# Kernel tuning notes

Measured on AMD Instinct MI355X. Metric: run time of the kernel, lower is better.

Reference implementation:

```python
import jax, jax.numpy as jnp
import numpy as np
from jax import lax

EPS = 1e-5  # BatchNorm eps (inference mode: running_mean=m, running_var=v)
DN = ('NCDHW', 'OIDHW', 'NCDHW')


def _conv_bn_relu(x, W, b, g, bt, m, v, pad):
    y = lax.conv_general_dilated(x, W, window_strides=(1, 1, 1), padding=pad,
                                 dimension_numbers=DN)
    y = y + b[None, :, None, None, None]
    scale = g / jnp.sqrt(v + EPS)
    y = (y - m[None, :, None, None, None]) * scale[None, :, None, None, None] \
        + bt[None, :, None, None, None]
    return jax.nn.relu(y)


def _cal_patt(k, q, v):
    # spatial non-local attention over H*W, independently per (n, c, d)
    N, C, D, H, W = q.shape
    qf = q.reshape(N, C, D, H * W)
    kf = k.reshape(N, C, D, H * W)
    vf = v.reshape(N, C, D, H * W)
    # sigma[n,c,d,i,j] = q_i * k_j ; softmax over j ; out[j] = sum_i v_i * r_ij
    sigma = qf[..., :, None] * kf[..., None, :]          # [N,C,D,HW,HW]
    r = jax.nn.softmax(sigma, axis=-1)
    out = jnp.einsum('ncdi,ncdij->ncdj', vf, r)
    return out.reshape(N, C, D, H, W)


def _cal_datt(k, q, v):
    # temporal non-local attention over D, independently per (n, c, h, w)
    N, C, D, H, W = q.shape
    qf = jnp.transpose(q, (0, 1, 3, 4, 2))               # [N,C,H,W,D]
    kf = jnp.transpose(k, (0, 1, 3, 4, 2))
    vf = jnp.transpose(v, (0, 1, 3, 4, 2))
    sigma = qf[..., :, None] * kf[..., None, :]          # [N,C,H,W,D,D]
    r = jax.nn.softmax(sigma, axis=-1)
    out = jnp.einsum('nchwi,nchwij->nchwj', vf, r)
    return jnp.transpose(out, (0, 1, 4, 2, 3))           # back to [N,C,D,H,W]


def setup_inputs() -> dict:
    key = jax.random.key(0)
    ks = jax.random.split(key, 8)
    C, Cc = 512, 64  # features_, features_//compress
    N, D, H, W = 2, 8, 16, 16
    f32 = jnp.float32

    def bn(c):
        return (jnp.ones((c,), f32), jnp.zeros((c,), f32),
                jnp.zeros((c,), f32), jnp.ones((c,), f32))

    x = jax.random.normal(ks[0], (N, C, D, H, W), f32)
    Wq = jax.random.normal(ks[1], (Cc, C, 1, 1, 1), f32) * 0.04
    Wk = jax.random.normal(ks[2], (Cc, C, 1, 1, 1), f32) * 0.04
    Wv = jax.random.normal(ks[3], (Cc, C, 1, 1, 1), f32) * 0.04
    Ws = jax.random.normal(ks[4], (C, Cc, 3, 3, 3), f32) * 0.02
    Wd = jax.random.normal(ks[5], (C, Cc, 3, 3, 3), f32) * 0.02
    gq, btq, mq, vq = bn(Cc)
    gk, btk, mk, vk = bn(Cc)
    gv, btv, mv, vv = bn(Cc)
    gs, bts, ms, vs = bn(C)
    gd, btd, md, vd = bn(C)
    return dict(
        x=x, gama=jnp.float32(0.5),
        Wq=Wq, bq=jnp.zeros((Cc,), f32), gq=gq, btq=btq, mq=mq, vq=vq,
        Wk=Wk, bk=jnp.zeros((Cc,), f32), gk=gk, btk=btk, mk=mk, vk=vk,
        Wv=Wv, bv=jnp.zeros((Cc,), f32), gv=gv, btv=btv, mv=mv, vv=vv,
        Ws=Ws, bs=jnp.zeros((C,), f32), gs=gs, bts=bts, ms=ms, vs=vs,
        Wd=Wd, bd=jnp.zeros((C,), f32), gd=gd, btd=btd, md=md, vd=vd,
    )


def reference(x, gama,
              Wq, bq, gq, btq, mq, vq,
              Wk, bk, gk, btk, mk, vk,
              Wv, bv, gv, btv, mv, vv,
              Ws, bs, gs, bts, ms, vs,
              Wd, bd, gd, btd, md, vd):
    P0 = [(0, 0)] * 3
    P1 = [(1, 1)] * 3
    v_x = _conv_bn_relu(x, Wv, bv, gv, btv, mv, vv, P0)
    k_x = _conv_bn_relu(x, Wk, bk, gk, btk, mk, vk, P0)
    q_x = _conv_bn_relu(x, Wq, bq, gq, btq, mq, vq, P0)
    # name == 'st': both spatial and temporal attention branches
    Patt = _cal_patt(k_x, q_x, v_x)
    Patt_c = _conv_bn_relu(Patt, Ws, bs, gs, bts, ms, vs, P1)
    Datt = _cal_datt(k_x, q_x, v_x)
    Datt_c = _conv_bn_relu(Datt, Wd, bd, gd, btd, md, vd, P1)
    return gama * (Datt_c + Patt_c) + x
```

## Files before the change

kernel.cpp:

```cpp
#include <hip/hip_runtime.h>
#include <cmath>

#define EPSBN 1e-5f

namespace {
constexpr int C_IN = 512;
constexpr int CC   = 64;
constexpr int CD   = 8;
constexpr int HW   = 256;
constexpr int DHW  = CD * HW;
constexpr int QSZ  = 2 * CC * DHW;

constexpr int PG    = 18 * 18;
constexpr int GPLN  = PG * 8;
constexpr int PADSZ = 2 * 10 * 8 * GPLN;
constexpr int WTSZ  = 27 * 512 * 64;

typedef __attribute__((ext_vector_type(8))) short bf16x8;
typedef __attribute__((ext_vector_type(4))) float f32x4;
typedef __attribute__((ext_vector_type(16))) float f32x16;

typedef unsigned int u32_g __attribute__((address_space(1)));
typedef unsigned int u32_l __attribute__((address_space(3)));

__device__ inline unsigned short f2bf(float f) {
    unsigned u = __float_as_uint(f);
    return (unsigned short)((u + 0x7fffu + ((u >> 16) & 1u)) >> 16);
}
}

__global__ __launch_bounds__(256) void prep_kernel(
    const float* __restrict__ Ws, const float* __restrict__ Wd,
    const float* __restrict__ Wq, const float* __restrict__ Wk,
    const float* __restrict__ Wv,
    const float* __restrict__ bs, const float* __restrict__ gs,
    const float* __restrict__ bts, const float* __restrict__ ms,
    const float* __restrict__ vs,
    const float* __restrict__ bd, const float* __restrict__ gd,
    const float* __restrict__ btd, const float* __restrict__ md,
    const float* __restrict__ vd,
    uint4* __restrict__ pads, unsigned short* __restrict__ Wt,
    unsigned short* __restrict__ Wqkv, float2* __restrict__ BNc)
{
    int bid = blockIdx.x;
    int t = threadIdx.x;
    if (bid < 405) {
        pads[bid * 256 + t] = make_uint4(0, 0, 0, 0);
    } else if (bid < 1429) {
        int b2 = bid - 405;
        int b  = b2 >> 9;
        int co = b2 & 511;
        const float* W = b ? Wd : Ws;
        int cog = co >> 6, co_l = co & 63;
        int r  = co_l & 31, hi = co_l >> 5;
        unsigned short* o = Wt + (size_t)b * WTSZ;
        for (int k = t; k < 27 * 64; k += 256) {
            int tap = k >> 6, ci = k & 63;
            int kd = tap / 9, tapk = tap - kd * 9;
            int half = ci >> 5, cl = ci & 31;
            int cig = cl >> 4, ci16 = cl & 15;
            int ks = ci16 >> 3;
            float w = W[((size_t)co * 64 + ci) * 27 + tap];
            int chunk = ((cog * 2 + half) * 3 + kd) * 2 + cig;
            int pg = (r * 2 + ks) ^ (r & 7);
            o[(size_t)chunk * 9216 + tapk * 1024 + hi * 512
              + pg * 8 + (ci16 & 7)] = f2bf(w);
        }
    } else if (bid < 1621) {
        int co = bid - 1429;
        const float* W = co < 64 ? Wq : co < 128 ? Wk : Wv;
        int c = co & 63;
        for (int ci = t; ci < 512; ci += 256)
            Wqkv[(size_t)co * 512 + ci] = f2bf(W[(size_t)c * 512 + ci]);
    } else {
        int gid = (bid - 1621) * 256 + t;
        if (gid < 1024) {
            int br = gid >> 9, co = gid & 511;
            float s, o;
            if (br == 0) {
                s = gs[co] * rsqrtf(vs[co] + EPSBN);
                o = (bs[co] - ms[co]) * s + bts[co];
            } else {
                s = gd[co] * rsqrtf(vd[co] + EPSBN);
                o = (bd[co] - md[co]) * s + btd[co];
            }
            BNc[gid] = make_float2(s, o);
        }
    }
}

__global__ __launch_bounds__(256) void qkv_gemm_kernel(
    const float* __restrict__ x, const unsigned short* __restrict__ Wqkv,
    const float* __restrict__ bq, const float* __restrict__ gq,
    const float* __restrict__ btq, const float* __restrict__ mq,
    const float* __restrict__ vq,
    const float* __restrict__ bk, const float* __restrict__ gk,
    const float* __restrict__ btk, const float* __restrict__ mk,
    const float* __restrict__ vk,
    const float* __restrict__ bv, const float* __restrict__ gv,
    const float* __restrict__ btv, const float* __restrict__ mv,
    const float* __restrict__ vv,
    float* __restrict__ outq, float* __restrict__ outk, float* __restrict__ outv)
{
    int bid = blockIdx.x;
    int n = bid >> 7, p0 = (bid & 127) * 16;

    __shared__ __align__(16) unsigned short xs[16 * 512];
    int t = threadIdx.x;

    const float* xb = x + ((size_t)n * C_IN) * DHW + p0;
#pragma unroll
    for (int pass = 0; pass < 8; ++pass) {
        int idx = pass * 256 + t;
        int ci = idx >> 2, pq = idx & 3;
        float4 v4 = *reinterpret_cast<const float4*>(xb + (size_t)ci * DHW + pq * 4);
        float arr[4] = {v4.x, v4.y, v4.z, v4.w};
#pragma unroll
        for (int u = 0; u < 4; ++u) {
            int pos = pq * 4 + u;
            int boff = pos * 1024 + ((ci * 2) ^ ((pos & 7) << 4));
            *reinterpret_cast<unsigned short*>(
                reinterpret_cast<char*>(xs) + boff) = f2bf(arr[u]);
        }
    }
    __syncthreads();

    int wid = t >> 6, lane = t & 63;
    int l15 = lane & 15, l4 = lane >> 4;
    int mh = wid * 3;
    int pos = l15;

    bf16x8 bfr[16];
    const char* xsb = reinterpret_cast<const char*>(xs) + pos * 1024;
    int swz = (pos & 7) << 4;
#pragma unroll
    for (int kk = 0; kk < 16; ++kk)
        bfr[kk] = *reinterpret_cast<const bf16x8*>(xsb + ((kk * 64 + l4 * 16) ^ swz));

    f32x4 acc[3];
#pragma unroll
    for (int i = 0; i < 3; ++i) acc[i] = (f32x4){0.f, 0.f, 0.f, 0.f};

#pragma unroll
    for (int i = 0; i < 3; ++i) {
        const unsigned short* wrow =
            Wqkv + ((size_t)(mh + i) * 16 + l15) * 512 + l4 * 8;
#pragma unroll
        for (int kk = 0; kk < 16; ++kk) {
            bf16x8 af = *reinterpret_cast<const bf16x8*>(wrow + kk * 32);
            acc[i] = __builtin_amdgcn_mfma_f32_16x16x32_bf16(af, bfr[kk], acc[i], 0, 0, 0);
        }
    }

#pragma unroll
    for (int i = 0; i < 3; ++i) {
        int mf = mh + i;
        int br = mf >> 2;
        const float* bb  = br == 0 ? bq  : br == 1 ? bk  : bv;
        const float* gg  = br == 0 ? gq  : br == 1 ? gk  : gv;
        const float* bt  = br == 0 ? btq : br == 1 ? btk : btv;
        const float* mm  = br == 0 ? mq  : br == 1 ? mk  : mv;
        const float* vvp = br == 0 ? vq  : br == 1 ? vk  : vv;
        float*       op  = br == 0 ? outq : br == 1 ? outk : outv;
        int cb = (mf & 3) * 16 + l4 * 4;
#pragma unroll
        for (int r = 0; r < 4; ++r) {
            int c = cb + r;
            float s = gg[c] * rsqrtf(vvp[c] + EPSBN);
            float val = (acc[i][r] + bb[c] - mm[c]) * s + bt[c];
            op[((size_t)(n * CC + c)) * DHW + p0 + pos] = fmaxf(val, 0.f);
        }
    }
}

__global__ __launch_bounds__(256) void att_kernel(
    const float* __restrict__ q, const float* __restrict__ k,
    const float* __restrict__ v,
    unsigned short* __restrict__ Pp, unsigned short* __restrict__ Dp)
{
    __shared__ float sk[256], sq[256], sw[256], red[4];
    int t = threadIdx.x;
    int bid = blockIdx.x;

    if (bid < 1024) {
        int n = bid >> 9, c = (bid >> 3) & 63, d = bid & 7;
        size_t base = (size_t)bid * HW;
        float kt = k[base + t];
        float qt = q[base + t];
        float vt = v[base + t];
        sk[t] = kt;
        sq[t] = qt;

        float m = kt;
#pragma unroll
        for (int off = 32; off >= 1; off >>= 1)
            m = fmaxf(m, __shfl_xor(m, off));
        if ((t & 63) == 0) red[t >> 6] = m;
        __syncthreads();
        float kmax = fmaxf(fmaxf(red[0], red[1]), fmaxf(red[2], red[3]));

        float qkm = qt * kmax;
        float d0 = 0.f, d1 = 0.f, d2 = 0.f, d3 = 0.f;
        for (int j = 0; j < 256; j += 4) {
            d0 += __expf(fmaf(qt, sk[j + 0], -qkm));
            d1 += __expf(fmaf(qt, sk[j + 1], -qkm));
            d2 += __expf(fmaf(qt, sk[j + 2], -qkm));
            d3 += __expf(fmaf(qt, sk[j + 3], -qkm));
        }
        float den = (d0 + d1) + (d2 + d3);
        sw[t] = vt / den;
        __syncthreads();

        float kjm = kt - kmax;
        float o0 = 0.f, o1 = 0.f, o2 = 0.f, o3 = 0.f;
        for (int i = 0; i < 256; i += 4) {
            o0 += sw[i + 0] * __expf(sq[i + 0] * kjm);
            o1 += sw[i + 1] * __expf(sq[i + 1] * kjm);
            o2 += sw[i + 2] * __expf(sq[i + 2] * kjm);
            o3 += sw[i + 3] * __expf(sq[i + 3] * kjm);
        }
        float o = (o0 + o1) + (o2 + o3);

        int h = t >> 4, w = t & 15;
        size_t dst = ((((size_t)(n * 10 + d + 1) * 8 + (c >> 3)) * PG)
                      + (h + 1) * 18 + (w + 1)) * 8 + (c & 7);
        Pp[dst] = f2bf(o);
    } else {
        int g = (bid - 1024) * 256 + t;
        int nc = g >> 8, hw = g & 255;
        int n = nc >> 6, c = nc & 63;
        size_t base = (size_t)nc * DHW + hw;

        float qv[8], kv[8], vv_[8];
#pragma unroll
        for (int d = 0; d < 8; ++d) {
            qv[d]  = q[base + d * HW];
            kv[d]  = k[base + d * HW];
            vv_[d] = v[base + d * HW];
        }
        float kmax = 0.f;
#pragma unroll
        for (int d = 0; d < 8; ++d) kmax = fmaxf(kmax, kv[d]);

        float wgt[8];
#pragma unroll
        for (int i = 0; i < 8; ++i) {
            float den = 0.f, qkm = qv[i] * kmax;
#pragma unroll
            for (int j = 0; j < 8; ++j)
                den += __expf(fmaf(qv[i], kv[j], -qkm));
            wgt[i] = vv_[i] / den;
        }
        int h = hw >> 4, w = hw & 15;
#pragma unroll
        for (int j = 0; j < 8; ++j) {
            float o = 0.f, kjm = kv[j] - kmax;
#pragma unroll
            for (int i = 0; i < 8; ++i)
                o += wgt[i] * __expf(qv[i] * kjm);
            size_t dst = ((((size_t)(n * 10 + j + 1) * 8 + (c >> 3)) * PG)
                          + (h + 1) * 18 + (w + 1)) * 8 + (c & 7);
            Dp[dst] = f2bf(o);
        }
    }
}

__global__ __launch_bounds__(256, 1) void conv_fused_kernel(
    const unsigned short* __restrict__ Pp, const unsigned short* __restrict__ Dp,
    const unsigned short* __restrict__ Wt,
    const float2* __restrict__ BNc,
    const float* __restrict__ x, const float* __restrict__ gama,
    float* __restrict__ out)
{
    int bid = blockIdx.x;
    int cog = bid & 7;
    int pgb = (bid >> 3) & 1;
    int sl  = bid >> 4;
    int n = sl >> 3, d = sl & 7;

    __shared__ __align__(16) unsigned short lds_in[24 * 1536];
    __shared__ __align__(16) unsigned short lds_w[2 * 18432];

    int t = threadIdx.x;
    int wid = t >> 6, lane = t & 63;
    int ph = wid & 1, br = wid >> 1;
    int col  = lane & 31;
    int wcol = lane & 15;
    int hl   = (lane >> 4) & 1;
    int ks   = lane >> 5;
    int gA   = ((col * 2 + ks) ^ (col & 7)) * 8;

    f32x16 acc[2][2];
#pragma unroll
    for (int m = 0; m < 2; ++m)
#pragma unroll
        for (int p = 0; p < 2; ++p)
#pragma unroll
            for (int r = 0; r < 16; ++r)
                acc[m][p][r] = 0.f;

#define ISTAGE(hf_) do {                                                      \
    _Pragma("unroll")                                                         \
    for (int pc = 0; pc < 24; ++pc) {                                         \
        const unsigned short* sb = ((pc >= 12) ? Dp : Pp)                     \
            + ((size_t)((n * 10 + d + ((pc % 12) >> 2)) * 8 + (hf_) * 4       \
                        + ((pc % 12) & 3))) * GPLN + pgb * 1152;              \
        _Pragma("unroll")                                                     \
        for (int j = 0; j < 3; ++j) {                                         \
            if (((pc * 3 + j) & 3) == wid)                                    \
                __builtin_amdgcn_global_load_lds(                             \
                    (const u32_g*)(sb + j * 512 + lane * 8),                  \
                    (u32_l*)(lds_in + pc * 1536 + j * 512), 16, 0, 0);        \
        }                                                                     \
    }                                                                         \
} while (0)

#define DMAW(c_) do {                                                         \
    const int ch_ = (((cog * 2 + ((c_) / 6)) * 3 + (((c_) % 6) >> 1)) * 2     \
                     + ((c_) & 1)) * 9216;                                    \
    _Pragma("unroll")                                                         \
    for (int j = 0; j < 9; ++j) {                                             \
        int base = j * 2048 + wid * 512;                                      \
        const unsigned short* s0 = (base < 9216)                              \
            ? (Wt + ch_ + base)                                               \
            : (Wt + WTSZ + ch_ + (base - 9216));                              \
        __builtin_amdgcn_global_load_lds(                                     \
            (const u32_g*)(s0 + lane * 8),                                    \
            (u32_l*)(lds_w + ((c_) & 1) * 18432 + base), 16, 0, 0);           \
    }                                                                         \
} while (0)

#define COMPUTE(c_) do {                                                      \
    const int kd_ = ((c_) % 6) >> 1, cig_ = (c_) & 1;                         \
    const unsigned short* wb_ = lds_w + ((c_) & 1) * 18432 + br * 9216;       \
    const unsigned short* bp_ = lds_in + br * (12 * 1536)                     \
                                + (kd_ * 4 + cig_ * 2 + ks) * 1536;           \
    _Pragma("unroll")                                                         \
    for (int tapk = 0; tapk < 9; ++tapk) {                                    \
        const int kh_ = tapk / 3, kw_ = tapk % 3;                             \
        bf16x8 a0 = *(const bf16x8*)(wb_ + tapk * 1024 + gA);                 \
        bf16x8 a1 = *(const bf16x8*)(wb_ + tapk * 1024 + 512 + gA);           \
        bf16x8 b0 = *(const bf16x8*)(bp_ + ((ph * 4 + hl + kh_) * 18          \
                                     + wcol + kw_) * 8);                      \
        bf16x8 b1 = *(const bf16x8*)(bp_ + ((ph * 4 + 2 + hl + kh_) * 18      \
                                     + wcol + kw_) * 8);                      \
        acc[0][0] = __builtin_amdgcn_mfma_f32_32x32x16_bf16(a0, b0,           \
                        acc[0][0], 0, 0, 0);                                  \
        acc[0][1] = __builtin_amdgcn_mfma_f32_32x32x16_bf16(a0, b1,           \
                        acc[0][1], 0, 0, 0);                                  \
        acc[1][0] = __builtin_amdgcn_mfma_f32_32x32x16_bf16(a1, b0,           \
                        acc[1][0], 0, 0, 0);                                  \
        acc[1][1] = __builtin_amdgcn_mfma_f32_32x32x16_bf16(a1, b1,           \
                        acc[1][1], 0, 0, 0);                                  \
    }                                                                         \
} while (0)

    ISTAGE(0);
    DMAW(0);
    __syncthreads();

#pragma unroll
    for (int c = 0; c < 12; ++c) {
        if (c < 11) DMAW(c + 1);
        COMPUTE(c);
        __syncthreads();
        if (c == 5) {
            ISTAGE(1);
            __syncthreads();
        }
    }

#undef ISTAGE
#undef DMAW
#undef COMPUTE

    float gm = gama[0];
    float* ep = reinterpret_cast<float*>(lds_w);

    if (br == 0) {
#pragma unroll
        for (int m = 0; m < 2; ++m)
#pragma unroll
            for (int p = 0; p < 2; ++p)
#pragma unroll
                for (int r = 0; r < 16; ++r) {
                    int row = (r & 3) + 8 * (r >> 2) + 4 * ks;
                    float2 c2 = BNc[cog * 64 + m * 32 + row];
                    float v = fmaxf(acc[m][p][r] * c2.x + c2.y, 0.f);
                    ep[ph * 4096 + (m * 32 + row) * 64 + p * 32 + col] = v;
                }
    }
    __syncthreads();
    if (br == 1) {
#pragma unroll
        for (int m = 0; m < 2; ++m)
#pragma unroll
            for (int p = 0; p < 2; ++p)
#pragma unroll
                for (int r = 0; r < 16; ++r) {
                    int row = (r & 3) + 8 * (r >> 2) + 4 * ks;
                    int co = cog * 64 + m * 32 + row;
                    float2 c2 = BNc[512 + co];
                    float rd = fmaxf(acc[m][p][r] * c2.x + c2.y, 0.f);
                    float rp = ep[ph * 4096 + (m * 32 + row) * 64 + p * 32 + col];
                    int pos = pgb * 128 + ph * 64 + p * 32 + col;
                    size_t oi = ((size_t)(n * 512 + co)) * 2048 + d * 256 + pos;
                    out[oi] = gm * (rp + rd) + x[oi];
                }
    }
}

extern "C" void kernel_launch(void* const* d_in, const int* in_sizes, int n_in,
                              void* d_out, int out_size, void* d_ws, size_t ws_size,
                              hipStream_t stream)
{
    const float* x    = (const float*)d_in[0];
    const float* gama = (const float*)d_in[1];
    const float* Wq  = (const float*)d_in[2];
    const float* bq  = (const float*)d_in[3];
    const float* gq  = (const float*)d_in[4];
    const float* btq = (const float*)d_in[5];
    const float* mq  = (const float*)d_in[6];
    const float* vq  = (const float*)d_in[7];
    const float* Wk  = (const float*)d_in[8];
    const float* bk  = (const float*)d_in[9];
    const float* gk  = (const float*)d_in[10];
    const float* btk = (const float*)d_in[11];
    const float* mk  = (const float*)d_in[12];
    const float* vk  = (const float*)d_in[13];
    const float* Wv  = (const float*)d_in[14];
    const float* bv  = (const float*)d_in[15];
    const float* gv  = (const float*)d_in[16];
    const float* btv = (const float*)d_in[17];
    const float* mv  = (const float*)d_in[18];
    const float* vv  = (const float*)d_in[19];
    const float* Ws  = (const float*)d_in[20];
    const float* bs  = (const float*)d_in[21];
    const float* gs  = (const float*)d_in[22];
    const float* bts = (const float*)d_in[23];
    const float* ms  = (const float*)d_in[24];
    const float* vs  = (const float*)d_in[25];
    const float* Wd  = (const float*)d_in[26];
    const float* bd  = (const float*)d_in[27];
    const float* gd  = (const float*)d_in[28];
    const float* btd = (const float*)d_in[29];
    const float* md  = (const float*)d_in[30];
    const float* vd  = (const float*)d_in[31];

    char* ws = (char*)d_ws;
    unsigned short* Pp   = (unsigned short*)ws;
    unsigned short* Dp   = Pp + PADSZ;
    unsigned short* Wt   = Dp + PADSZ;
    unsigned short* Wqkv = Wt + 2 * WTSZ;
    float* q = (float*)(ws + 5394432);
    float* k = q + QSZ;
    float* v = k + QSZ;
    float2* BNc = (float2*)(ws + 5394432 + 3 * 1048576);

    prep_kernel<<<1625, 256, 0, stream>>>(
        Ws, Wd, Wq, Wk, Wv,
        bs, gs, bts, ms, vs,
        bd, gd, btd, md, vd,
        (uint4*)Pp, Wt, Wqkv, BNc);

    qkv_gemm_kernel<<<256, 256, 0, stream>>>(
        x, Wqkv,
        bq, gq, btq, mq, vq,
        bk, gk, btk, mk, vk,
        bv, gv, btv, mv, vv,
        q, k, v);

    att_kernel<<<1152, 256, 0, stream>>>(q, k, v, Pp, Dp);

    conv_fused_kernel<<<256, 256, 0, stream>>>(
        Pp, Dp, Wt, BNc,
        x, gama, (float*)d_out);
}
```

Before: 65.02 us.

## Double-buffer conv input staging per chunk and vectorize attention LDS reads

The fused conv kernel no longer stages a whole half of the input planes (24 planes) at once with an extra barrier mid-loop. It now double-buffers a small 4-plane input slice per chunk alongside the weight DMA, which shrinks LDS use from about 72KB to 24KB for inputs and removes the stall at chunk 5. The attention kernel reads its shared k/q/w arrays as float4 with partial unrolling, and the weight-prep loop now reads source weights contiguously. The risk is more frequent small DMA issues per iteration, which could add latency if the per-chunk loads are not hidden behind compute.

```diff
diff --git a/kernel.cpp b/kernel.cpp
--- a/kernel.cpp
+++ b/kernel.cpp
@@ -54,13 +54,14 @@
         int cog = co >> 6, co_l = co & 63;
         int r  = co_l & 31, hi = co_l >> 5;
         unsigned short* o = Wt + (size_t)b * WTSZ;
-        for (int k = t; k < 27 * 64; k += 256) {
-            int tap = k >> 6, ci = k & 63;
+        for (int k2 = t; k2 < 27 * 64; k2 += 256) {
+            int ci  = k2 / 27;
+            int tap = k2 - ci * 27;
             int kd = tap / 9, tapk = tap - kd * 9;
             int half = ci >> 5, cl = ci & 31;
             int cig = cl >> 4, ci16 = cl & 15;
             int ks = ci16 >> 3;
-            float w = W[((size_t)co * 64 + ci) * 27 + tap];
+            float w = W[(size_t)co * 1728 + k2];
             int chunk = ((cog * 2 + half) * 3 + kd) * 2 + cig;
             int pg = (r * 2 + ks) ^ (r & 7);
             o[(size_t)chunk * 9216 + tapk * 1024 + hi * 512
@@ -178,7 +179,8 @@
     const float* __restrict__ v,
     unsigned short* __restrict__ Pp, unsigned short* __restrict__ Dp)
 {
-    __shared__ float sk[256], sq[256], sw[256], red[4];
+    __shared__ __align__(16) float sk[256], sq[256], sw[256];
+    __shared__ float red[4];
     int t = threadIdx.x;
     int bid = blockIdx.x;
 
@@ -201,11 +203,14 @@
 
         float qkm = qt * kmax;
         float d0 = 0.f, d1 = 0.f, d2 = 0.f, d3 = 0.f;
-        for (int j = 0; j < 256; j += 4) {
-            d0 += __expf(fmaf(qt, sk[j + 0], -qkm));
-            d1 += __expf(fmaf(qt, sk[j + 1], -qkm));
-            d2 += __expf(fmaf(qt, sk[j + 2], -qkm));
-            d3 += __expf(fmaf(qt, sk[j + 3], -qkm));
+        const float4* sk4 = reinterpret_cast<const float4*>(sk);
+#pragma unroll 8
+        for (int j = 0; j < 64; ++j) {
+            float4 kk = sk4[j];
+            d0 += __expf(fmaf(qt, kk.x, -qkm));
+            d1 += __expf(fmaf(qt, kk.y, -qkm));
+            d2 += __expf(fmaf(qt, kk.z, -qkm));
+            d3 += __expf(fmaf(qt, kk.w, -qkm));
         }
         float den = (d0 + d1) + (d2 + d3);
         sw[t] = vt / den;
@@ -213,11 +218,16 @@
 
         float kjm = kt - kmax;
         float o0 = 0.f, o1 = 0.f, o2 = 0.f, o3 = 0.f;
-        for (int i = 0; i < 256; i += 4) {
-            o0 += sw[i + 0] * __expf(sq[i + 0] * kjm);
-            o1 += sw[i + 1] * __expf(sq[i + 1] * kjm);
-            o2 += sw[i + 2] * __expf(sq[i + 2] * kjm);
-            o3 += sw[i + 3] * __expf(sq[i + 3] * kjm);
+        const float4* sw4 = reinterpret_cast<const float4*>(sw);
+        const float4* sq4 = reinterpret_cast<const float4*>(sq);
+#pragma unroll 8
+        for (int i = 0; i < 64; ++i) {
+            float4 ww = sw4[i];
+            float4 qq = sq4[i];
+            o0 += ww.x * __expf(qq.x * kjm);
+            o1 += ww.y * __expf(qq.y * kjm);
+            o2 += ww.z * __expf(qq.z * kjm);
+            o3 += ww.w * __expf(qq.w * kjm);
         }
         float o = (o0 + o1) + (o2 + o3);
 
@@ -278,7 +288,7 @@
     int sl  = bid >> 4;
     int n = sl >> 3, d = sl & 7;
 
-    __shared__ __align__(16) unsigned short lds_in[24 * 1536];
+    __shared__ __align__(16) unsigned short lds_i[8 * 1536];
     __shared__ __align__(16) unsigned short lds_w[2 * 18432];
 
     int t = threadIdx.x;
@@ -299,18 +309,21 @@
             for (int r = 0; r < 16; ++r)
                 acc[m][p][r] = 0.f;
 
-#define ISTAGE(hf_) do {                                                      \
+#define DMAI(c_) do {                                                         \
+    const int half_ = (c_) / 6, kd_ = (((c_) % 6) >> 1), cig_ = (c_) & 1;     \
     _Pragma("unroll")                                                         \
-    for (int pc = 0; pc < 24; ++pc) {                                         \
-        const unsigned short* sb = ((pc >= 12) ? Dp : Pp)                     \
-            + ((size_t)((n * 10 + d + ((pc % 12) >> 2)) * 8 + (hf_) * 4       \
-                        + ((pc % 12) & 3))) * GPLN + pgb * 1152;              \
+    for (int pc = 0; pc < 4; ++pc) {                                          \
+        const int br_ = pc >> 1, ks_ = pc & 1;                                \
+        const unsigned short* sb = (br_ ? Dp : Pp)                            \
+            + ((size_t)((n * 10 + d + kd_) * 8 + half_ * 4 + cig_ * 2 + ks_)) \
+              * GPLN + pgb * 1152;                                            \
         _Pragma("unroll")                                                     \
         for (int j = 0; j < 3; ++j) {                                         \
             if (((pc * 3 + j) & 3) == wid)                                    \
                 __builtin_amdgcn_global_load_lds(                             \
                     (const u32_g*)(sb + j * 512 + lane * 8),                  \
-                    (u32_l*)(lds_in + pc * 1536 + j * 512), 16, 0, 0);        \
+                    (u32_l*)(lds_i + (((c_) & 1) * 4 + pc) * 1536 + j * 512), \
+                    16, 0, 0);                                                \
         }                                                                     \
     }                                                                         \
 } while (0)
@@ -331,10 +344,8 @@
 } while (0)
 
 #define COMPUTE(c_) do {                                                      \
-    const int kd_ = ((c_) % 6) >> 1, cig_ = (c_) & 1;                         \
     const unsigned short* wb_ = lds_w + ((c_) & 1) * 18432 + br * 9216;       \
-    const unsigned short* bp_ = lds_in + br * (12 * 1536)                     \
-                                + (kd_ * 4 + cig_ * 2 + ks) * 1536;           \
+    const unsigned short* bp_ = lds_i + (((c_) & 1) * 4 + br * 2 + ks) * 1536;\
     _Pragma("unroll")                                                         \
     for (int tapk = 0; tapk < 9; ++tapk) {                                    \
         const int kh_ = tapk / 3, kw_ = tapk % 3;                             \
@@ -355,22 +366,21 @@
     }                                                                         \
 } while (0)
 
-    ISTAGE(0);
+    DMAI(0);
     DMAW(0);
     __syncthreads();
 
 #pragma unroll
     for (int c = 0; c < 12; ++c) {
-        if (c < 11) DMAW(c + 1);
+        if (c < 11) {
+            DMAW(c + 1);
+            DMAI(c + 1);
+        }
         COMPUTE(c);
         __syncthreads();
-        if (c == 5) {
-            ISTAGE(1);
-            __syncthreads();
-        }
-    }
-
-#undef ISTAGE
+    }
+
+#undef DMAI
 #undef DMAW
 #undef COMPUTE
 
```

Measured after the change: 67.56 us. 1.04x slower.

## Fuse weight prep and QKV GEMM into one head kernel, relax conv barriers

Applied to the files above, without the earlier changes.

Merges the prep and QKV projection kernels into a single launch. The QKV blocks now read the fp32 Wq/Wk/Wv weights directly and convert them to bf16 in registers, so the intermediate Wqkv buffer and one kernel launch go away. The conv weight repack loop is reordered so its global reads are contiguous. The conv pipeline replaces __syncthreads with raw s_barrier plus explicit vmcnt waits so that the next chunk's DMA can stay in flight. The risks are redundant weight conversion in every block and the correctness of the hand-tuned vmcnt count.

```diff
diff --git a/kernel.cpp b/kernel.cpp
--- a/kernel.cpp
+++ b/kernel.cpp
@@ -29,10 +29,20 @@
 }
 }
 
-__global__ __launch_bounds__(256) void prep_kernel(
-    const float* __restrict__ Ws, const float* __restrict__ Wd,
+__global__ __launch_bounds__(256) void head_kernel(
+    const float* __restrict__ x,
     const float* __restrict__ Wq, const float* __restrict__ Wk,
     const float* __restrict__ Wv,
+    const float* __restrict__ bq, const float* __restrict__ gq,
+    const float* __restrict__ btq, const float* __restrict__ mq,
+    const float* __restrict__ vq,
+    const float* __restrict__ bk, const float* __restrict__ gk,
+    const float* __restrict__ btk, const float* __restrict__ mk,
+    const float* __restrict__ vk,
+    const float* __restrict__ bv, const float* __restrict__ gv,
+    const float* __restrict__ btv, const float* __restrict__ mv,
+    const float* __restrict__ vv,
+    const float* __restrict__ Ws, const float* __restrict__ Wd,
     const float* __restrict__ bs, const float* __restrict__ gs,
     const float* __restrict__ bts, const float* __restrict__ ms,
     const float* __restrict__ vs,
@@ -40,40 +50,114 @@
     const float* __restrict__ btd, const float* __restrict__ md,
     const float* __restrict__ vd,
     uint4* __restrict__ pads, unsigned short* __restrict__ Wt,
-    unsigned short* __restrict__ Wqkv, float2* __restrict__ BNc)
+    float2* __restrict__ BNc,
+    float* __restrict__ outq, float* __restrict__ outk, float* __restrict__ outv)
 {
     int bid = blockIdx.x;
     int t = threadIdx.x;
-    if (bid < 405) {
-        pads[bid * 256 + t] = make_uint4(0, 0, 0, 0);
-    } else if (bid < 1429) {
-        int b2 = bid - 405;
+
+    if (bid < 256) {
+        int n = bid >> 7, p0 = (bid & 127) * 16;
+
+        __shared__ __align__(16) unsigned short xs[16 * 512];
+
+        const float* xb = x + ((size_t)n * C_IN) * DHW + p0;
+#pragma unroll
+        for (int pass = 0; pass < 8; ++pass) {
+            int idx = pass * 256 + t;
+            int ci = idx >> 2, pq = idx & 3;
+            float4 v4 = *reinterpret_cast<const float4*>(xb + (size_t)ci * DHW + pq * 4);
+            float arr[4] = {v4.x, v4.y, v4.z, v4.w};
+#pragma unroll
+            for (int u = 0; u < 4; ++u) {
+                int pos = pq * 4 + u;
+                int boff = pos * 1024 + ((ci * 2) ^ ((pos & 7) << 4));
+                *reinterpret_cast<unsigned short*>(
+                    reinterpret_cast<char*>(xs) + boff) = f2bf(arr[u]);
+            }
+        }
+        __syncthreads();
+
+        int wid = t >> 6, lane = t & 63;
+        int l15 = lane & 15, l4 = lane >> 4;
+        int mh = wid * 3;
+        int pos = l15;
+
+        bf16x8 bfr[16];
+        const char* xsb = reinterpret_cast<const char*>(xs) + pos * 1024;
+        int swz = (pos & 7) << 4;
+#pragma unroll
+        for (int kk = 0; kk < 16; ++kk)
+            bfr[kk] = *reinterpret_cast<const bf16x8*>(xsb + ((kk * 64 + l4 * 16) ^ swz));
+
+        f32x4 acc[3];
+#pragma unroll
+        for (int i = 0; i < 3; ++i) acc[i] = (f32x4){0.f, 0.f, 0.f, 0.f};
+
+#pragma unroll
+        for (int i = 0; i < 3; ++i) {
+            int mf = mh + i;
+            int br = mf >> 2;
+            const float* Wsel = br == 0 ? Wq : br == 1 ? Wk : Wv;
+            int c = (mf & 3) * 16 + l15;
+            const float* wr = Wsel + (size_t)c * 512 + l4 * 8;
+#pragma unroll
+            for (int kk = 0; kk < 16; ++kk) {
+                float4 wa = *reinterpret_cast<const float4*>(wr + kk * 32);
+                float4 wb = *reinterpret_cast<const float4*>(wr + kk * 32 + 4);
+                bf16x8 af;
+                af[0] = (short)f2bf(wa.x); af[1] = (short)f2bf(wa.y);
+                af[2] = (short)f2bf(wa.z); af[3] = (short)f2bf(wa.w);
+                af[4] = (short)f2bf(wb.x); af[5] = (short)f2bf(wb.y);
+                af[6] = (short)f2bf(wb.z); af[7] = (short)f2bf(wb.w);
+                acc[i] = __builtin_amdgcn_mfma_f32_16x16x32_bf16(af, bfr[kk], acc[i], 0, 0, 0);
+            }
+        }
+
+#pragma unroll
+        for (int i = 0; i < 3; ++i) {
+            int mf = mh + i;
+            int br = mf >> 2;
+            const float* bb  = br == 0 ? bq  : br == 1 ? bk  : bv;
+            const float* gg  = br == 0 ? gq  : br == 1 ? gk  : gv;
+            const float* bt  = br == 0 ? btq : br == 1 ? btk : btv;
+            const float* mm  = br == 0 ? mq  : br == 1 ? mk  : mv;
+            const float* vvp = br == 0 ? vq  : br == 1 ? vk  : vv;
+            float*       op  = br == 0 ? outq : br == 1 ? outk : outv;
+            int cb = (mf & 3) * 16 + l4 * 4;
+#pragma unroll
+            for (int r = 0; r < 4; ++r) {
+                int c = cb + r;
+                float s = gg[c] * rsqrtf(vvp[c] + EPSBN);
+                float val = (acc[i][r] + bb[c] - mm[c]) * s + bt[c];
+                op[((size_t)(n * CC + c)) * DHW + p0 + pos] = fmaxf(val, 0.f);
+            }
+        }
+    } else if (bid < 661) {
+        pads[(bid - 256) * 256 + t] = make_uint4(0, 0, 0, 0);
+    } else if (bid < 1685) {
+        int b2 = bid - 661;
         int b  = b2 >> 9;
         int co = b2 & 511;
         const float* W = b ? Wd : Ws;
         int cog = co >> 6, co_l = co & 63;
         int r  = co_l & 31, hi = co_l >> 5;
         unsigned short* o = Wt + (size_t)b * WTSZ;
-        for (int k = t; k < 27 * 64; k += 256) {
-            int tap = k >> 6, ci = k & 63;
+        for (int k2 = t; k2 < 27 * 64; k2 += 256) {
+            int ci  = k2 / 27;
+            int tap = k2 - ci * 27;
             int kd = tap / 9, tapk = tap - kd * 9;
             int half = ci >> 5, cl = ci & 31;
             int cig = cl >> 4, ci16 = cl & 15;
             int ks = ci16 >> 3;
-            float w = W[((size_t)co * 64 + ci) * 27 + tap];
+            float w = W[(size_t)co * 1728 + k2];
             int chunk = ((cog * 2 + half) * 3 + kd) * 2 + cig;
             int pg = (r * 2 + ks) ^ (r & 7);
             o[(size_t)chunk * 9216 + tapk * 1024 + hi * 512
               + pg * 8 + (ci16 & 7)] = f2bf(w);
         }
-    } else if (bid < 1621) {
-        int co = bid - 1429;
-        const float* W = co < 64 ? Wq : co < 128 ? Wk : Wv;
-        int c = co & 63;
-        for (int ci = t; ci < 512; ci += 256)
-            Wqkv[(size_t)co * 512 + ci] = f2bf(W[(size_t)c * 512 + ci]);
     } else {
-        int gid = (bid - 1621) * 256 + t;
+        int gid = (bid - 1685) * 256 + t;
         if (gid < 1024) {
             int br = gid >> 9, co = gid & 511;
             float s, o;
@@ -85,90 +169,6 @@
                 o = (bd[co] - md[co]) * s + btd[co];
             }
             BNc[gid] = make_float2(s, o);
-        }
-    }
-}
-
-__global__ __launch_bounds__(256) void qkv_gemm_kernel(
-    const float* __restrict__ x, const unsigned short* __restrict__ Wqkv,
-    const float* __restrict__ bq, const float* __restrict__ gq,
-    const float* __restrict__ btq, const float* __restrict__ mq,
-    const float* __restrict__ vq,
-    const float* __restrict__ bk, const float* __restrict__ gk,
-    const float* __restrict__ btk, const float* __restrict__ mk,
-    const float* __restrict__ vk,
-    const float* __restrict__ bv, const float* __restrict__ gv,
-    const float* __restrict__ btv, const float* __restrict__ mv,
-    const float* __restrict__ vv,
-    float* __restrict__ outq, float* __restrict__ outk, float* __restrict__ outv)
-{
-    int bid = blockIdx.x;
-    int n = bid >> 7, p0 = (bid & 127) * 16;
-
-    __shared__ __align__(16) unsigned short xs[16 * 512];
-    int t = threadIdx.x;
-
-    const float* xb = x + ((size_t)n * C_IN) * DHW + p0;
-#pragma unroll
-    for (int pass = 0; pass < 8; ++pass) {
-        int idx = pass * 256 + t;
-        int ci = idx >> 2, pq = idx & 3;
-        float4 v4 = *reinterpret_cast<const float4*>(xb + (size_t)ci * DHW + pq * 4);
-        float arr[4] = {v4.x, v4.y, v4.z, v4.w};
-#pragma unroll
-        for (int u = 0; u < 4; ++u) {
-            int pos = pq * 4 + u;
-            int boff = pos * 1024 + ((ci * 2) ^ ((pos & 7) << 4));
-            *reinterpret_cast<unsigned short*>(
-                reinterpret_cast<char*>(xs) + boff) = f2bf(arr[u]);
-        }
-    }
-    __syncthreads();
-
-    int wid = t >> 6, lane = t & 63;
-    int l15 = lane & 15, l4 = lane >> 4;
-    int mh = wid * 3;
-    int pos = l15;
-
-    bf16x8 bfr[16];
-    const char* xsb = reinterpret_cast<const char*>(xs) + pos * 1024;
-    int swz = (pos & 7) << 4;
-#pragma unroll
-    for (int kk = 0; kk < 16; ++kk)
-        bfr[kk] = *reinterpret_cast<const bf16x8*>(xsb + ((kk * 64 + l4 * 16) ^ swz));
-
-    f32x4 acc[3];
-#pragma unroll
-    for (int i = 0; i < 3; ++i) acc[i] = (f32x4){0.f, 0.f, 0.f, 0.f};
-
-#pragma unroll
-    for (int i = 0; i < 3; ++i) {
-        const unsigned short* wrow =
-            Wqkv + ((size_t)(mh + i) * 16 + l15) * 512 + l4 * 8;
-#pragma unroll
-        for (int kk = 0; kk < 16; ++kk) {
-            bf16x8 af = *reinterpret_cast<const bf16x8*>(wrow + kk * 32);
-            acc[i] = __builtin_amdgcn_mfma_f32_16x16x32_bf16(af, bfr[kk], acc[i], 0, 0, 0);
-        }
-    }
-
-#pragma unroll
-    for (int i = 0; i < 3; ++i) {
-        int mf = mh + i;
-        int br = mf >> 2;
-        const float* bb  = br == 0 ? bq  : br == 1 ? bk  : bv;
-        const float* gg  = br == 0 ? gq  : br == 1 ? gk  : gv;
-        const float* bt  = br == 0 ? btq : br == 1 ? btk : btv;
-        const float* mm  = br == 0 ? mq  : br == 1 ? mk  : mv;
-        const float* vvp = br == 0 ? vq  : br == 1 ? vk  : vv;
-        float*       op  = br == 0 ? outq : br == 1 ? outk : outv;
-        int cb = (mf & 3) * 16 + l4 * 4;
-#pragma unroll
-        for (int r = 0; r < 4; ++r) {
-            int c = cb + r;
-            float s = gg[c] * rsqrtf(vvp[c] + EPSBN);
-            float val = (acc[i][r] + bb[c] - mm[c]) * s + bt[c];
-            op[((size_t)(n * CC + c)) * DHW + p0 + pos] = fmaxf(val, 0.f);
         }
     }
 }
@@ -357,16 +357,22 @@
 
     ISTAGE(0);
     DMAW(0);
-    __syncthreads();
 
 #pragma unroll
     for (int c = 0; c < 12; ++c) {
-        if (c < 11) DMAW(c + 1);
+        if (c > 0)
+            __builtin_amdgcn_s_barrier();
+        if (c < 11) {
+            DMAW(c + 1);
+            asm volatile("s_waitcnt vmcnt(9)" ::: "memory");
+        } else {
+            asm volatile("s_waitcnt vmcnt(0)" ::: "memory");
+        }
+        __builtin_amdgcn_s_barrier();
         COMPUTE(c);
-        __syncthreads();
         if (c == 5) {
+            __builtin_amdgcn_s_barrier();
             ISTAGE(1);
-            __syncthreads();
         }
     }
 
@@ -451,23 +457,21 @@
     unsigned short* Pp   = (unsigned short*)ws;
     unsigned short* Dp   = Pp + PADSZ;
     unsigned short* Wt   = Dp + PADSZ;
-    unsigned short* Wqkv = Wt + 2 * WTSZ;
     float* q = (float*)(ws + 5394432);
     float* k = q + QSZ;
     float* v = k + QSZ;
     float2* BNc = (float2*)(ws + 5394432 + 3 * 1048576);
 
-    prep_kernel<<<1625, 256, 0, stream>>>(
-        Ws, Wd, Wq, Wk, Wv,
-        bs, gs, bts, ms, vs,
-        bd, gd, btd, md, vd,
-        (uint4*)Pp, Wt, Wqkv, BNc);
-
-    qkv_gemm_kernel<<<256, 256, 0, stream>>>(
-        x, Wqkv,
+    head_kernel<<<1689, 256, 0, stream>>>(
+        x,
+        Wq, Wk, Wv,
         bq, gq, btq, mq, vq,
         bk, gk, btk, mk, vk,
         bv, gv, btv, mv, vv,
+        Ws, Wd,
+        bs, gs, bts, ms, vs,
+        bd, gd, btd, md, vd,
+        (uint4*)Pp, Wt, BNc,
         q, k, v);
 
     att_kernel<<<1152, 256, 0, stream>>>(q, k, v, Pp, Dp);
```

Result: slower. 67.96 us (+4.5%).

## Double conv block to 512 threads, splitting positions across more waves

Applied to the files above, without the earlier changes.

The fused 3x3x3 conv kernel now runs with 8 waves per block instead of 4. Each wave computes one 32-position quarter with two MFMA accumulators instead of a 2x2 tile, and the input and weight DMA loops are redistributed across the 8 waves. This aims to improve latency hiding and MFMA issue parallelism on each CU with only 256 blocks, at the cost of reloading the A fragments in more waves and adding sync overhead. The weight prep loop is also changed to read the source weights contiguously.

```diff
diff --git a/kernel.cpp b/kernel.cpp
--- a/kernel.cpp
+++ b/kernel.cpp
@@ -54,13 +54,14 @@
         int cog = co >> 6, co_l = co & 63;
         int r  = co_l & 31, hi = co_l >> 5;
         unsigned short* o = Wt + (size_t)b * WTSZ;
-        for (int k = t; k < 27 * 64; k += 256) {
-            int tap = k >> 6, ci = k & 63;
+        for (int k2 = t; k2 < 27 * 64; k2 += 256) {
+            int ci  = k2 / 27;
+            int tap = k2 - ci * 27;
             int kd = tap / 9, tapk = tap - kd * 9;
             int half = ci >> 5, cl = ci & 31;
             int cig = cl >> 4, ci16 = cl & 15;
             int ks = ci16 >> 3;
-            float w = W[((size_t)co * 64 + ci) * 27 + tap];
+            float w = W[(size_t)co * 1728 + k2];
             int chunk = ((cog * 2 + half) * 3 + kd) * 2 + cig;
             int pg = (r * 2 + ks) ^ (r & 7);
             o[(size_t)chunk * 9216 + tapk * 1024 + hi * 512
@@ -265,7 +266,7 @@
     }
 }
 
-__global__ __launch_bounds__(256, 1) void conv_fused_kernel(
+__global__ __launch_bounds__(512, 1) void conv_fused_kernel(
     const unsigned short* __restrict__ Pp, const unsigned short* __restrict__ Dp,
     const unsigned short* __restrict__ Wt,
     const float2* __restrict__ BNc,
@@ -283,21 +284,19 @@
 
     int t = threadIdx.x;
     int wid = t >> 6, lane = t & 63;
-    int ph = wid & 1, br = wid >> 1;
+    int posq = wid & 3, br = wid >> 2;
     int col  = lane & 31;
     int wcol = lane & 15;
     int hl   = (lane >> 4) & 1;
     int ks   = lane >> 5;
     int gA   = ((col * 2 + ks) ^ (col & 7)) * 8;
 
-    f32x16 acc[2][2];
+    f32x16 acc[2];
 #pragma unroll
     for (int m = 0; m < 2; ++m)
 #pragma unroll
-        for (int p = 0; p < 2; ++p)
-#pragma unroll
-            for (int r = 0; r < 16; ++r)
-                acc[m][p][r] = 0.f;
+        for (int r = 0; r < 16; ++r)
+            acc[m][r] = 0.f;
 
 #define ISTAGE(hf_) do {                                                      \
     _Pragma("unroll")                                                         \
@@ -307,7 +306,7 @@
                         + ((pc % 12) & 3))) * GPLN + pgb * 1152;              \
         _Pragma("unroll")                                                     \
         for (int j = 0; j < 3; ++j) {                                         \
-            if (((pc * 3 + j) & 3) == wid)                                    \
+            if (((pc * 3 + j) & 7) == wid)                                    \
                 __builtin_amdgcn_global_load_lds(                             \
                     (const u32_g*)(sb + j * 512 + lane * 8),                  \
                     (u32_l*)(lds_in + pc * 1536 + j * 512), 16, 0, 0);        \
@@ -319,14 +318,16 @@
     const int ch_ = (((cog * 2 + ((c_) / 6)) * 3 + (((c_) % 6) >> 1)) * 2     \
                      + ((c_) & 1)) * 9216;                                    \
     _Pragma("unroll")                                                         \
-    for (int j = 0; j < 9; ++j) {                                             \
-        int base = j * 2048 + wid * 512;                                      \
-        const unsigned short* s0 = (base < 9216)                              \
-            ? (Wt + ch_ + base)                                               \
-            : (Wt + WTSZ + ch_ + (base - 9216));                              \
-        __builtin_amdgcn_global_load_lds(                                     \
-            (const u32_g*)(s0 + lane * 8),                                    \
-            (u32_l*)(lds_w + ((c_) & 1) * 18432 + base), 16, 0, 0);           \
+    for (int j = 0; j < 5; ++j) {                                             \
+        int base = j * 4096 + wid * 512;                                      \
+        if (base < 18432) {                                                   \
+            const unsigned short* s0 = (base < 9216)                          \
+                ? (Wt + ch_ + base)                                           \
+                : (Wt + WTSZ + ch_ + (base - 9216));                          \
+            __builtin_amdgcn_global_load_lds(                                 \
+                (const u32_g*)(s0 + lane * 8),                                \
+                (u32_l*)(lds_w + ((c_) & 1) * 18432 + base), 16, 0, 0);       \
+        }                                                                     \
     }                                                                         \
 } while (0)
 
@@ -340,18 +341,12 @@
         const int kh_ = tapk / 3, kw_ = tapk % 3;                             \
         bf16x8 a0 = *(const bf16x8*)(wb_ + tapk * 1024 + gA);                 \
         bf16x8 a1 = *(const bf16x8*)(wb_ + tapk * 1024 + 512 + gA);           \
-        bf16x8 b0 = *(const bf16x8*)(bp_ + ((ph * 4 + hl + kh_) * 18          \
+        bf16x8 b0 = *(const bf16x8*)(bp_ + ((posq * 2 + hl + kh_) * 18        \
                                      + wcol + kw_) * 8);                      \
-        bf16x8 b1 = *(const bf16x8*)(bp_ + ((ph * 4 + 2 + hl + kh_) * 18      \
-                                     + wcol + kw_) * 8);                      \
-        acc[0][0] = __builtin_amdgcn_mfma_f32_32x32x16_bf16(a0, b0,           \
-                        acc[0][0], 0, 0, 0);                                  \
-        acc[0][1] = __builtin_amdgcn_mfma_f32_32x32x16_bf16(a0, b1,           \
-                        acc[0][1], 0, 0, 0);                                  \
-        acc[1][0] = __builtin_amdgcn_mfma_f32_32x32x16_bf16(a1, b0,           \
-                        acc[1][0], 0, 0, 0);                                  \
-        acc[1][1] = __builtin_amdgcn_mfma_f32_32x32x16_bf16(a1, b1,           \
-                        acc[1][1], 0, 0, 0);                                  \
+        acc[0] = __builtin_amdgcn_mfma_f32_32x32x16_bf16(a0, b0,              \
+                     acc[0], 0, 0, 0);                                        \
+        acc[1] = __builtin_amdgcn_mfma_f32_32x32x16_bf16(a1, b0,              \
+                     acc[1], 0, 0, 0);                                        \
     }                                                                         \
 } while (0)
 
@@ -381,32 +376,28 @@
 #pragma unroll
         for (int m = 0; m < 2; ++m)
 #pragma unroll
-            for (int p = 0; p < 2; ++p)
-#pragma unroll
-                for (int r = 0; r < 16; ++r) {
-                    int row = (r & 3) + 8 * (r >> 2) + 4 * ks;
-                    float2 c2 = BNc[cog * 64 + m * 32 + row];
-                    float v = fmaxf(acc[m][p][r] * c2.x + c2.y, 0.f);
-                    ep[ph * 4096 + (m * 32 + row) * 64 + p * 32 + col] = v;
-                }
+            for (int r = 0; r < 16; ++r) {
+                int row = (r & 3) + 8 * (r >> 2) + 4 * ks;
+                float2 c2 = BNc[cog * 64 + m * 32 + row];
+                float v = fmaxf(acc[m][r] * c2.x + c2.y, 0.f);
+                ep[posq * 2048 + (m * 32 + row) * 32 + col] = v;
+            }
     }
     __syncthreads();
     if (br == 1) {
 #pragma unroll
         for (int m = 0; m < 2; ++m)
 #pragma unroll
-            for (int p = 0; p < 2; ++p)
-#pragma unroll
-                for (int r = 0; r < 16; ++r) {
-                    int row = (r & 3) + 8 * (r >> 2) + 4 * ks;
-                    int co = cog * 64 + m * 32 + row;
-                    float2 c2 = BNc[512 + co];
-                    float rd = fmaxf(acc[m][p][r] * c2.x + c2.y, 0.f);
-                    float rp = ep[ph * 4096 + (m * 32 + row) * 64 + p * 32 + col];
-                    int pos = pgb * 128 + ph * 64 + p * 32 + col;
-                    size_t oi = ((size_t)(n * 512 + co)) * 2048 + d * 256 + pos;
-                    out[oi] = gm * (rp + rd) + x[oi];
-                }
+            for (int r = 0; r < 16; ++r) {
+                int row = (r & 3) + 8 * (r >> 2) + 4 * ks;
+                int co = cog * 64 + m * 32 + row;
+                float2 c2 = BNc[512 + co];
+                float rd = fmaxf(acc[m][r] * c2.x + c2.y, 0.f);
+                float rp = ep[posq * 2048 + (m * 32 + row) * 32 + col];
+                int pos = pgb * 128 + posq * 32 + col;
+                size_t oi = ((size_t)(n * 512 + co)) * 2048 + d * 256 + pos;
+                out[oi] = gm * (rp + rd) + x[oi];
+            }
     }
 }
 
@@ -472,7 +463,7 @@
 
     att_kernel<<<1152, 256, 0, stream>>>(q, k, v, Pp, Dp);
 
-    conv_fused_kernel<<<256, 256, 0, stream>>>(
+    conv_fused_kernel<<<256, 512, 0, stream>>>(
         Pp, Dp, Wt, BNc,
         x, gama, (float*)d_out);
 }
```

After: 67.25 us. 3.4% more time.
